# Optimization experiments

Measured on AMD Instinct MI355X. Metric: run time of the kernel, lower is better.

## Reference

```python
import jax, jax.numpy as jnp
import numpy as np

D_MODEL = 1024
N_HEADS = 16
D_HEAD = 64
D_FF = 4096
BATCH = 4
SEQ = 2048
EPS = 1e-05


def gelu_lean(x):
    cubic = x * x * x
    cdf = 0.5 * (1.0 + jnp.tanh(0.7978845608 * (x + 0.044715 * cubic)))
    return x * cdf


def layernorm(x, gamma, beta):
    mean = jnp.mean(x, axis=-1, keepdims=True)
    var = jnp.mean((x - mean) ** 2, axis=-1, keepdims=True)
    return gamma * ((x - mean) / jnp.sqrt(var + EPS)) + beta


def setup_inputs() -> dict:
    key = jax.random.key(0)
    ks = jax.random.split(key, 8)
    std = 0.02
    return {
        "x": jax.random.normal(ks[0], (BATCH, SEQ, D_MODEL), dtype=jnp.float32),
        "gamma1": jnp.ones((D_MODEL,), jnp.float32),
        "beta1": jnp.zeros((D_MODEL,), jnp.float32),
        "wq": std * jax.random.normal(ks[1], (N_HEADS, D_HEAD, D_MODEL), dtype=jnp.float32),
        "wk": std * jax.random.normal(ks[2], (N_HEADS, D_HEAD, D_MODEL), dtype=jnp.float32),
        "wv": std * jax.random.normal(ks[3], (N_HEADS, D_HEAD, D_MODEL), dtype=jnp.float32),
        "wo": std * jax.random.normal(ks[4], (D_MODEL, N_HEADS * D_HEAD), dtype=jnp.float32),
        "gamma2": jnp.ones((D_MODEL,), jnp.float32),
        "beta2": jnp.zeros((D_MODEL,), jnp.float32),
        "mlp_fc1": std * jax.random.normal(ks[5], (D_FF, D_MODEL), dtype=jnp.float32),
        "mlp_fc2": std * jax.random.normal(ks[6], (D_MODEL, D_FF), dtype=jnp.float32),
    }


def reference(x, gamma1, beta1, wq, wk, wv, wo, gamma2, beta2, mlp_fc1, mlp_fc2):
    n = layernorm(x, gamma1, beta1)  # [B,S,D]
    scale = jnp.sqrt(jnp.float32(D_HEAD))
    # per-head projections, vectorized over heads: [B,S,H,dh]
    q = jnp.einsum("bsd,hed->bshe", n, wq)
    k = jnp.einsum("bsd,hed->bshe", n, wk)
    v = jnp.einsum("bsd,hed->bshe", n, wv)
    scores = jnp.einsum("bqhe,bkhe->bhqk", q, k) / scale  # [B,H,S,S]
    seq = x.shape[1]
    mask = jnp.triu(jnp.ones((seq, seq), dtype=bool), k=1)
    scores = jnp.where(mask, jnp.float32(-1e9), scores)
    weights = jax.nn.softmax(scores, axis=-1)
    attn = jnp.einsum("bhqk,bkhe->bqhe", weights, v)  # [B,S,H,dh]
    concat = attn.reshape(x.shape[0], seq, N_HEADS * D_HEAD)  # head-order concat
    attn_out = concat @ wo.T
    x_resid = x + attn_out
    n2 = layernorm(x_resid, gamma2, beta2)
    hidden = gelu_lean(n2 @ mlp_fc1.T)
    mlp_out = hidden @ mlp_fc2.T
    return x_resid + mlp_out
```

## Files before the change

### kernel.cpp

```cpp
#include <hip/hip_runtime.h>
#include <hip/hip_bf16.h>

#define D_MODEL 1024
#define N_HEADS 16
#define D_HEAD  64
#define D_FF    4096
#define BATCH   4
#define SEQ     2048
#define ROWS    (BATCH*SEQ)
#define LN_EPS  1e-5f

typedef __bf16 bf16;
typedef __bf16 bf16x8 __attribute__((ext_vector_type(8)));
typedef float  f32x4  __attribute__((ext_vector_type(4)));

__device__ __forceinline__ void load16_lds(const bf16* g, bf16* l) {
#if defined(__has_builtin) && __has_builtin(__builtin_amdgcn_global_load_lds)
    __builtin_amdgcn_global_load_lds(
        (const __attribute__((address_space(1))) unsigned int*)g,
        (__attribute__((address_space(3))) unsigned int*)l,
        16, 0, 0);
#else
    const int lane = threadIdx.x & 63;
    ((bf16x8*)l)[lane] = *(const bf16x8*)g;
#endif
}

__global__ __launch_bounds__(256) void f2b4_kernel(const float* a, const float* b,
                                                   const float* c, const float* d,
                                                   bf16* oa, bf16* ob, bf16* oc, bf16* od,
                                                   int n) {
    const float* srcs[4] = {a, b, c, d};
    bf16* dsts[4] = {oa, ob, oc, od};
    const float* s = srcs[blockIdx.y];
    bf16* dst = dsts[blockIdx.y];
    int i = blockIdx.x * 256 + threadIdx.x;
    int stride = gridDim.x * 256;
    for (; i < n; i += stride) dst[i] = (bf16)s[i];
}
__global__ __launch_bounds__(256) void f2b2_kernel(const float* a, const float* b,
                                                   bf16* oa, bf16* ob, int n) {
    const float* s = blockIdx.y ? b : a;
    bf16* dst = blockIdx.y ? ob : oa;
    int i = blockIdx.x * 256 + threadIdx.x;
    int stride = gridDim.x * 256;
    for (; i < n; i += stride) dst[i] = (bf16)s[i];
}

__global__ __launch_bounds__(256) void ln_kernel(const float* __restrict__ x,
                                                 const float* __restrict__ gamma,
                                                 const float* __restrict__ beta,
                                                 bf16* __restrict__ out) {
    const int row = blockIdx.x;
    const int tid = threadIdx.x;
    const float* xr = x + (size_t)row * D_MODEL;

    float vals[4];
    float s = 0.f, ss = 0.f;
#pragma unroll
    for (int t = 0; t < 4; ++t) {
        float v = xr[tid + t * 256];
        vals[t] = v;
        s += v;
        ss += v * v;
    }
#pragma unroll
    for (int off = 32; off > 0; off >>= 1) {
        s  += __shfl_xor(s, off, 64);
        ss += __shfl_xor(ss, off, 64);
    }
    __shared__ float sbuf[4], ssbuf[4];
    const int wave = tid >> 6;
    if ((tid & 63) == 0) { sbuf[wave] = s; ssbuf[wave] = ss; }
    __syncthreads();
    s  = sbuf[0] + sbuf[1] + sbuf[2] + sbuf[3];
    ss = ssbuf[0] + ssbuf[1] + ssbuf[2] + ssbuf[3];

    const float mean = s * (1.f / D_MODEL);
    const float var  = ss * (1.f / D_MODEL) - mean * mean;
    const float inv  = rsqrtf(var + LN_EPS);

    bf16* orow = out + (size_t)row * D_MODEL;
#pragma unroll
    for (int t = 0; t < 4; ++t) {
        int c = tid + t * 256;
        orow[c] = (bf16)(gamma[c] * ((vals[t] - mean) * inv) + beta[c]);
    }
}

__device__ __forceinline__ float gelu_f(float x) {
    const float y = x * (0.7978845608f + 0.0356774081f * x * x);
    return x / (1.f + __expf(-2.f * y));
}

template <int EPI, int TN, int BK, typename OutT>
__global__ __launch_bounds__(256) void gemm_mt(const bf16* __restrict__ A,
                                               const bf16* __restrict__ W,
                                               OutT* C,
                                               const float* ADD,
                                               bf16* VT,
                                               int M, int N, int K, int LDK) {
    constexpr int WN = TN / 64;
    constexpr int WM = 4 / WN;
    constexpr int SM = (128 / WM) / 16;

    constexpr int AB_ELEMS = 128 * BK + TN * BK;
    constexpr int TB_ELEMS = (EPI == 4) ? 4 * 64 * 72 : 0;
    constexpr int SMEM_ELEMS = AB_ELEMS > TB_ELEMS ? AB_ELEMS : TB_ELEMS;
    __shared__ __align__(16) bf16 smem[SMEM_ELEMS];
    bf16* sA   = smem;
    bf16* sB   = smem + 128 * BK;
    bf16* tbuf = smem;

    const int wave = threadIdx.x >> 6;
    const int lane = threadIdx.x & 63;
    const int quad = lane >> 4;
    const int l16  = lane & 15;
    const int wm   = wave / WN;
    const int wn   = wave % WN;

    const int nN  = N / TN;
    const int b   = blockIdx.x;
    const int xcd = b & 7;
    const int j   = b >> 3;
    const int bx  = j % nN;
    const int band = (j / nN) * 8 + xcd;

    const int m0 = band * 128;
    const int n0 = bx * TN;

    f32x4 acc[SM][4] = {};

    if constexpr (BK == 32) {
        const int srow = lane >> 2;
        const int scol = (lane & 3) * 8;
        const bf16* gA0 = A + (size_t)(m0 + wave * 32 + srow) * LDK + scol;
        const bf16* gA1 = gA0 + (size_t)16 * LDK;
        bf16* lA0 = &sA[(wave * 32) * 32];
        bf16* lA1 = &sA[(wave * 32 + 16) * 32];
        const bf16* gB0 = W + (size_t)(n0 + wave * (TN / 4) + srow) * LDK + scol;
        const bf16* gB1 = gB0 + (size_t)16 * LDK;
        bf16* lB0 = &sB[(wave * (TN / 4)) * 32];
        bf16* lB1 = &sB[(wave * (TN / 4) + 16) * 32];

        for (int k0 = 0; k0 < K; k0 += 32) {
            load16_lds(gA0 + k0, lA0);
            load16_lds(gA1 + k0, lA1);
            load16_lds(gB0 + k0, lB0);
            if constexpr (TN == 128) load16_lds(gB1 + k0, lB1);
            __syncthreads();

            bf16x8 af[SM], bfr[4];
#pragma unroll
            for (int s = 0; s < SM; ++s)
                af[s] = *reinterpret_cast<const bf16x8*>(&sA[(wm * (128 / WM) + s * 16 + l16) * 32 + quad * 8]);
#pragma unroll
            for (int t = 0; t < 4; ++t)
                bfr[t] = *reinterpret_cast<const bf16x8*>(&sB[(wn * 64 + t * 16 + l16) * 32 + quad * 8]);
#pragma unroll
            for (int s = 0; s < SM; ++s)
#pragma unroll
                for (int t = 0; t < 4; ++t)
                    acc[s][t] = __builtin_amdgcn_mfma_f32_16x16x32_bf16(af[s], bfr[t], acc[s][t], 0, 0, 0);
            __syncthreads();
        }
    } else {
        const int lrow = lane >> 3;
        const int lch  = ((lane & 7) ^ lrow) * 8;
        const bf16* gA = A + (size_t)(m0 + wave * 32 + lrow) * LDK + lch;
        bf16* lA = &sA[(wave * 32) * 64];
        const bf16* gB = W + (size_t)(n0 + wave * (TN / 4) + lrow) * LDK + lch;
        bf16* lB = &sB[(wave * (TN / 4)) * 64];

        for (int k0 = 0; k0 < K; k0 += 64) {
#pragma unroll
            for (int i = 0; i < 4; ++i)
                load16_lds(gA + k0 + (size_t)(8 * i) * LDK, lA + 8 * i * 64);
#pragma unroll
            for (int i = 0; i < (TN / 4) / 8; ++i)
                load16_lds(gB + k0 + (size_t)(8 * i) * LDK, lB + 8 * i * 64);
            __syncthreads();

#pragma unroll
            for (int kk = 0; kk < 2; ++kk) {
                bf16x8 af[SM], bfr[4];
#pragma unroll
                for (int s = 0; s < SM; ++s) {
                    const int row = wm * (128 / WM) + s * 16 + l16;
                    const int sl  = (kk * 4 + quad) ^ (row & 7);
                    af[s] = *reinterpret_cast<const bf16x8*>(&sA[row * 64 + sl * 8]);
                }
#pragma unroll
                for (int t = 0; t < 4; ++t) {
                    const int row = wn * 64 + t * 16 + l16;
                    const int sl  = (kk * 4 + quad) ^ (row & 7);
                    bfr[t] = *reinterpret_cast<const bf16x8*>(&sB[row * 64 + sl * 8]);
                }
#pragma unroll
                for (int s = 0; s < SM; ++s)
#pragma unroll
                    for (int t = 0; t < 4; ++t)
                        acc[s][t] = __builtin_amdgcn_mfma_f32_16x16x32_bf16(af[s], bfr[t], acc[s][t], 0, 0, 0);
            }
            __syncthreads();
        }
    }

    if constexpr (EPI == 4) {
        if (n0 >= 2048) {
            bf16* tw = &tbuf[wave * 64 * 72];
#pragma unroll
            for (int s = 0; s < SM; ++s)
#pragma unroll
                for (int t = 0; t < 4; ++t)
#pragma unroll
                    for (int r = 0; r < 4; ++r)
                        tw[(t * 16 + l16) * 72 + s * 16 + quad * 4 + r] = (bf16)acc[s][t][r];
#pragma unroll
            for (int i = 0; i < 8; ++i) {
                const int flat = i * 64 + lane;
                const int nl = flat >> 3;
                const int mc = flat & 7;
                bf16x8 v = *reinterpret_cast<const bf16x8*>(&tw[nl * 72 + mc * 8]);
                const int vcol = n0 - 2048 + wn * 64 + nl;
                const int m_glob = m0 + wm * 64 + mc * 8;
                const int bb = m_glob >> 11, sp = m_glob & (SEQ - 1);
                const int hh = vcol >> 6,  dh = vcol & 63;
                const size_t tidx = (((size_t)(bb * N_HEADS + hh) * D_HEAD + dh) << 11) + sp;
                *reinterpret_cast<bf16x8*>(&VT[tidx]) = v;
            }
        } else {
            const float qscale = (n0 < 1024) ? 0.125f : 1.0f;
#pragma unroll
            for (int s = 0; s < SM; ++s) {
                const int mbase = m0 + wm * (128 / WM) + s * 16 + quad * 4;
#pragma unroll
                for (int t = 0; t < 4; ++t) {
                    const int n = n0 + wn * 64 + t * 16 + l16;
#pragma unroll
                    for (int r = 0; r < 4; ++r)
                        C[(size_t)(mbase + r) * 2048 + n] = (OutT)(acc[s][t][r] * qscale);
                }
            }
        }
    } else {
#pragma unroll
        for (int s = 0; s < SM; ++s) {
            const int mbase = m0 + wm * (128 / WM) + s * 16 + quad * 4;
#pragma unroll
            for (int t = 0; t < 4; ++t) {
                const int n = n0 + wn * 64 + t * 16 + l16;
#pragma unroll
                for (int r = 0; r < 4; ++r) {
                    float v = acc[s][t][r];
                    if (EPI == 1) v = gelu_f(v);
                    const size_t idx = (size_t)(mbase + r) * N + n;
                    if (EPI == 2) v += ADD[idx];
                    C[idx] = (OutT)v;
                }
            }
        }
    }
}

__global__ __launch_bounds__(256) void flash_attn_kernel(const bf16* __restrict__ qk,
                                                         const bf16* __restrict__ vt,
                                                         bf16* __restrict__ o) {
    const int id   = blockIdx.x;
    const int bhl  = id & 7;
    const int rest = id >> 3;
    const int pair = rest & 15;
    const int bhh  = rest >> 4;
    const int bh   = bhh * 8 + bhl;
    const int b    = bh >> 4;
    const int h    = bh & 15;
    const int wave = threadIdx.x >> 6;
    const int lane = threadIdx.x & 63;
    const int quad = lane >> 4;
    const int l16  = lane & 15;

    __shared__ __align__(16) bf16 sK[2][64 * 64];
    __shared__ __align__(16) bf16 sV[2][64 * 64];
    __shared__ bf16 pbuf[4][16][68];

    const bf16* kbase = qk + (size_t)(b * SEQ) * 2048 + 1024 + h * D_HEAD;
    const bf16* vbase = vt + ((size_t)(bh * D_HEAD) << 11);

    const int lrow   = lane >> 3;
    const int lchunk = (lane & 7) ^ lrow;
    const int xr     = l16 & 7;

    auto stage = [&](int j0, int buf) {
        const bf16* gk = kbase + (size_t)(j0 + wave * 16 + lrow) * 2048 + lchunk * 8;
        const bf16* gv = vbase + (size_t)(wave * 16 + lrow) * 2048 + j0 + lchunk * 8;
        load16_lds(gk,            &sK[buf][(wave * 16) * 64]);
        load16_lds(gk + 8 * 2048, &sK[buf][(wave * 16 + 8) * 64]);
        load16_lds(gv,            &sV[buf][(wave * 16) * 64]);
        load16_lds(gv + 8 * 2048, &sV[buf][(wave * 16 + 8) * 64]);
    };

    bf16x8 ones;
#pragma unroll
    for (int i = 0; i < 8; ++i) ones[i] = (bf16)1.0f;

    for (int half = 0; half < 2; ++half) {
        const int qtile = half ? 31 - pair : pair;
        const int q0 = qtile * 64 + wave * 16;
        const size_t qrow = (size_t)(b * SEQ + q0 + l16) * 2048 + h * D_HEAD;
        bf16x8 qf0 = *reinterpret_cast<const bf16x8*>(qk + qrow + quad * 8);
        bf16x8 qf1 = *reinterpret_cast<const bf16x8*>(qk + qrow + 32 + quad * 8);

        f32x4 o_acc[4] = {(f32x4)(0.f), (f32x4)(0.f), (f32x4)(0.f), (f32x4)(0.f)};
        float m_q = -1e30f;
        float l_r[4] = {0.f, 0.f, 0.f, 0.f};

        stage(0, 0);
        __syncthreads();

        for (int jt = 0; jt <= qtile; ++jt) {
            const int j0 = jt * 64;
            const int cur = jt & 1;
            if (jt < qtile) stage(j0 + 64, cur ^ 1);

            const bf16* sKc = sK[cur];
            const bf16* sVc = sV[cur];

            f32x4 s_acc[4] = {(f32x4)(0.f), (f32x4)(0.f), (f32x4)(0.f), (f32x4)(0.f)};
#pragma unroll
            for (int nb = 0; nb < 4; ++nb) {
                const int row = nb * 16 + l16;
                const int slot = quad ^ xr;
                bf16x8 kf0 = *reinterpret_cast<const bf16x8*>(&sKc[row * 64 + slot * 8]);
                bf16x8 kf1 = *reinterpret_cast<const bf16x8*>(&sKc[row * 64 + (slot ^ 4) * 8]);
                s_acc[nb] = __builtin_amdgcn_mfma_f32_16x16x32_bf16(qf0, kf0, s_acc[nb], 0, 0, 0);
                s_acc[nb] = __builtin_amdgcn_mfma_f32_16x16x32_bf16(qf1, kf1, s_acc[nb], 0, 0, 0);
            }
            const bool diag = (jt == qtile);
            float sv[4][4];
            float mx = -1e30f;
#pragma unroll
            for (int nb = 0; nb < 4; ++nb) {
                const int key = j0 + nb * 16 + l16;
#pragma unroll
                for (int r = 0; r < 4; ++r) {
                    float s = s_acc[nb][r];
                    if (diag && key > q0 + quad * 4 + r) s = -1e30f;
                    sv[nb][r] = s;
                    mx = fmaxf(mx, s);
                }
            }
#pragma unroll
            for (int off = 1; off < 16; off <<= 1) mx = fmaxf(mx, __shfl_xor(mx, off, 64));
            const float mn = fmaxf(m_q, mx);
            const float alpha = __expf(m_q - mn);
            m_q = mn;
#pragma unroll
            for (int nb = 0; nb < 4; ++nb)
#pragma unroll
                for (int r = 0; r < 4; ++r)
                    pbuf[wave][quad * 4 + r][nb * 16 + l16] = (bf16)__expf(sv[nb][r] - mn);
#pragma unroll
            for (int r = 0; r < 4; ++r) l_r[r] *= alpha;
#pragma unroll
            for (int nb = 0; nb < 4; ++nb) o_acc[nb] *= alpha;
            bf16x8 pf0 = *reinterpret_cast<const bf16x8*>(&pbuf[wave][l16][quad * 8]);
            bf16x8 pf1 = *reinterpret_cast<const bf16x8*>(&pbuf[wave][l16][32 + quad * 8]);
            f32x4 lt = (f32x4)(0.f);
            lt = __builtin_amdgcn_mfma_f32_16x16x32_bf16(pf0, ones, lt, 0, 0, 0);
            lt = __builtin_amdgcn_mfma_f32_16x16x32_bf16(pf1, ones, lt, 0, 0, 0);
#pragma unroll
            for (int r = 0; r < 4; ++r) l_r[r] += lt[r];
#pragma unroll
            for (int nb = 0; nb < 4; ++nb) {
                const int row = nb * 16 + l16;
                const int slot = quad ^ xr;
                bf16x8 vf0 = *reinterpret_cast<const bf16x8*>(&sVc[row * 64 + slot * 8]);
                bf16x8 vf1 = *reinterpret_cast<const bf16x8*>(&sVc[row * 64 + (slot ^ 4) * 8]);
                o_acc[nb] = __builtin_amdgcn_mfma_f32_16x16x32_bf16(pf0, vf0, o_acc[nb], 0, 0, 0);
                o_acc[nb] = __builtin_amdgcn_mfma_f32_16x16x32_bf16(pf1, vf1, o_acc[nb], 0, 0, 0);
            }
            __syncthreads();
        }
#pragma unroll
        for (int nb = 0; nb < 4; ++nb) {
#pragma unroll
            for (int r = 0; r < 4; ++r) {
                const int qrow_g = q0 + quad * 4 + r;
                o[(size_t)(b * SEQ + qrow_g) * D_MODEL + h * D_HEAD + nb * 16 + l16] =
                    (bf16)(o_acc[nb][r] / l_r[r]);
            }
        }
    }
}

extern "C" void kernel_launch(void* const* d_in, const int* in_sizes, int n_in,
                              void* d_out, int out_size, void* d_ws, size_t ws_size,
                              hipStream_t stream) {
    const float* x      = (const float*)d_in[0];
    const float* gamma1 = (const float*)d_in[1];
    const float* beta1  = (const float*)d_in[2];
    const float* wq     = (const float*)d_in[3];
    const float* wk     = (const float*)d_in[4];
    const float* wv     = (const float*)d_in[5];
    const float* wo     = (const float*)d_in[6];
    const float* gamma2 = (const float*)d_in[7];
    const float* beta2  = (const float*)d_in[8];
    const float* fc1    = (const float*)d_in[9];
    const float* fc2    = (const float*)d_in[10];
    float* out = (float*)d_out;

    const size_t WSMALL = (size_t)N_HEADS * D_HEAD * D_MODEL;
    const size_t WFF    = (size_t)D_FF * D_MODEL;
    const size_t RD     = (size_t)ROWS * D_MODEL;

    char* wsb = (char*)d_ws;
    bf16* wq_b  = (bf16*)(wsb);
    bf16* wk_b  = wq_b + WSMALL;
    bf16* wv_b  = wk_b + WSMALL;
    bf16* wo_b  = wv_b + WSMALL;
    bf16* fc1_b = wo_b + WSMALL;
    bf16* fc2_b = fc1_b + WFF;
    bf16* slotA = fc2_b + WFF;
    bf16* qkb   = slotA + RD;
    bf16* vtb   = qkb + 2 * RD;

    bf16* n1    = slotA;
    bf16* attnb = slotA;
    bf16* hid   = slotA;
    float* resid = out;

    const size_t need_single = (size_t)(24 + 64 + 16) * 1024 * 1024;
    const bool single = ws_size >= need_single;
    bf16* n2 = single ? (bf16*)(wsb + (size_t)88 * 1024 * 1024) : vtb;

    f2b4_kernel<<<dim3(64, 4), 256, 0, stream>>>(wq, wk, wv, wo, wq_b, wk_b, wv_b, wo_b, (int)WSMALL);
    f2b2_kernel<<<dim3(256, 2), 256, 0, stream>>>(fc1, fc2, fc1_b, fc2_b, (int)WFF);

    ln_kernel<<<ROWS, 256, 0, stream>>>(x, gamma1, beta1, n1);
    gemm_mt<4, 128, 64, bf16><<<(3072 / 128) * (ROWS / 128), 256, 0, stream>>>(n1, wq_b, qkb, nullptr, vtb, ROWS, 3072, D_MODEL, D_MODEL);
    flash_attn_kernel<<<1024, 256, 0, stream>>>(qkb, vtb, attnb);
    gemm_mt<2, 64, 64, float><<<(D_MODEL / 64) * (ROWS / 128), 256, 0, stream>>>(attnb, wo_b, resid, x, nullptr, ROWS, D_MODEL, D_MODEL, D_MODEL);
    ln_kernel<<<ROWS, 256, 0, stream>>>(resid, gamma2, beta2, n2);

    if (single) {
        gemm_mt<1, 128, 64, bf16><<<(D_FF / 128) * (ROWS / 128), 256, 0, stream>>>(n2, fc1_b, hid, nullptr, nullptr, ROWS, D_FF, D_MODEL, D_MODEL);
        gemm_mt<2, 64, 64, float><<<(D_MODEL / 64) * (ROWS / 128), 256, 0, stream>>>(hid, fc2_b, out, resid, nullptr, ROWS, D_MODEL, D_FF, D_FF);
    } else {
        const int CHUNK = 4096;
        for (int c = 0; c < ROWS / CHUNK; ++c) {
            const bf16*  n2c    = n2    + (size_t)c * CHUNK * D_MODEL;
            const float* residc = resid + (size_t)c * CHUNK * D_MODEL;
            float*       outc   = out   + (size_t)c * CHUNK * D_MODEL;
            gemm_mt<1, 128, 64, bf16><<<(D_FF / 128) * (CHUNK / 128), 256, 0, stream>>>(n2c, fc1_b, hid, nullptr, nullptr, CHUNK, D_FF, D_MODEL, D_MODEL);
            gemm_mt<2, 64, 64, float><<<(D_MODEL / 64) * (CHUNK / 128), 256, 0, stream>>>(hid, fc2_b, outc, residc, nullptr, CHUNK, D_MODEL, D_FF, D_FF);
        }
    }
}
```

Baseline: 546.9 us.

## Transpose attention MFMA so P stays in registers, dropping LDS round-trip

Swaps the MFMA operand order so S^T is computed, with each lane holding one query column. K rows are loaded into LDS in a permuted order so the accumulator layout matches the B-operand layout needed for the P·V MFMA. This removes the per-tile LDS write/read of P and the ones-MFMA used for row sums, which are replaced by register sums and two shuffles. Output is written as packed bf16x4 vectors. The cost is more complex index arithmetic for the causal mask and the permuted K staging.

New measurement: 527.6 us. 1.04x faster.

```diff
diff --git a/kernel.cpp b/kernel.cpp
--- a/kernel.cpp
+++ b/kernel.cpp
@@ -12,6 +12,7 @@
 
 typedef __bf16 bf16;
 typedef __bf16 bf16x8 __attribute__((ext_vector_type(8)));
+typedef __bf16 bf16x4 __attribute__((ext_vector_type(4)));
 typedef float  f32x4  __attribute__((ext_vector_type(4)));
 
 __device__ __forceinline__ void load16_lds(const bf16* g, bf16* l) {
@@ -281,7 +282,6 @@
 
     __shared__ __align__(16) bf16 sK[2][64 * 64];
     __shared__ __align__(16) bf16 sV[2][64 * 64];
-    __shared__ bf16 pbuf[4][16][68];
 
     const bf16* kbase = qk + (size_t)(b * SEQ) * 2048 + 1024 + h * D_HEAD;
     const bf16* vbase = vt + ((size_t)(bh * D_HEAD) << 11);
@@ -290,29 +290,31 @@
     const int lchunk = (lane & 7) ^ lrow;
     const int xr     = l16 & 7;
 
+    auto sig = [](int i) { return (i & 32) + (((i >> 2) & 3) << 3) + (((i >> 4) & 1) << 2) + (i & 3); };
+    const int sg0 = sig(wave * 16 + lrow);
+    const int sg1 = sig(wave * 16 + 8 + lrow);
+
     auto stage = [&](int j0, int buf) {
-        const bf16* gk = kbase + (size_t)(j0 + wave * 16 + lrow) * 2048 + lchunk * 8;
-        const bf16* gv = vbase + (size_t)(wave * 16 + lrow) * 2048 + j0 + lchunk * 8;
-        load16_lds(gk,            &sK[buf][(wave * 16) * 64]);
-        load16_lds(gk + 8 * 2048, &sK[buf][(wave * 16 + 8) * 64]);
+        const bf16* gk0 = kbase + (size_t)(j0 + sg0) * 2048 + lchunk * 8;
+        const bf16* gk1 = kbase + (size_t)(j0 + sg1) * 2048 + lchunk * 8;
+        const bf16* gv  = vbase + (size_t)(wave * 16 + lrow) * 2048 + j0 + lchunk * 8;
+        load16_lds(gk0, &sK[buf][(wave * 16) * 64]);
+        load16_lds(gk1, &sK[buf][(wave * 16 + 8) * 64]);
         load16_lds(gv,            &sV[buf][(wave * 16) * 64]);
         load16_lds(gv + 8 * 2048, &sV[buf][(wave * 16 + 8) * 64]);
     };
 
-    bf16x8 ones;
-#pragma unroll
-    for (int i = 0; i < 8; ++i) ones[i] = (bf16)1.0f;
-
     for (int half = 0; half < 2; ++half) {
         const int qtile = half ? 31 - pair : pair;
         const int q0 = qtile * 64 + wave * 16;
-        const size_t qrow = (size_t)(b * SEQ + q0 + l16) * 2048 + h * D_HEAD;
+        const int qg = q0 + l16;
+        const size_t qrow = (size_t)(b * SEQ + qg) * 2048 + h * D_HEAD;
         bf16x8 qf0 = *reinterpret_cast<const bf16x8*>(qk + qrow + quad * 8);
         bf16x8 qf1 = *reinterpret_cast<const bf16x8*>(qk + qrow + 32 + quad * 8);
 
         f32x4 o_acc[4] = {(f32x4)(0.f), (f32x4)(0.f), (f32x4)(0.f), (f32x4)(0.f)};
         float m_q = -1e30f;
-        float l_r[4] = {0.f, 0.f, 0.f, 0.f};
+        float l_r = 0.f;
 
         stage(0, 0);
         __syncthreads();
@@ -332,63 +334,77 @@
                 const int slot = quad ^ xr;
                 bf16x8 kf0 = *reinterpret_cast<const bf16x8*>(&sKc[row * 64 + slot * 8]);
                 bf16x8 kf1 = *reinterpret_cast<const bf16x8*>(&sKc[row * 64 + (slot ^ 4) * 8]);
-                s_acc[nb] = __builtin_amdgcn_mfma_f32_16x16x32_bf16(qf0, kf0, s_acc[nb], 0, 0, 0);
-                s_acc[nb] = __builtin_amdgcn_mfma_f32_16x16x32_bf16(qf1, kf1, s_acc[nb], 0, 0, 0);
-            }
+                s_acc[nb] = __builtin_amdgcn_mfma_f32_16x16x32_bf16(kf0, qf0, s_acc[nb], 0, 0, 0);
+                s_acc[nb] = __builtin_amdgcn_mfma_f32_16x16x32_bf16(kf1, qf1, s_acc[nb], 0, 0, 0);
+            }
+
             const bool diag = (jt == qtile);
-            float sv[4][4];
+            float p[4][4];
             float mx = -1e30f;
 #pragma unroll
             for (int nb = 0; nb < 4; ++nb) {
-                const int key = j0 + nb * 16 + l16;
 #pragma unroll
                 for (int r = 0; r < 4; ++r) {
                     float s = s_acc[nb][r];
-                    if (diag && key > q0 + quad * 4 + r) s = -1e30f;
-                    sv[nb][r] = s;
+                    if (diag) {
+                        const int key = j0 + ((nb & 2) << 4) + (quad << 3) + ((nb & 1) << 2) + r;
+                        if (key > qg) s = -1e30f;
+                    }
+                    p[nb][r] = s;
                     mx = fmaxf(mx, s);
                 }
             }
-#pragma unroll
-            for (int off = 1; off < 16; off <<= 1) mx = fmaxf(mx, __shfl_xor(mx, off, 64));
+            mx = fmaxf(mx, __shfl_xor(mx, 16, 64));
+            mx = fmaxf(mx, __shfl_xor(mx, 32, 64));
             const float mn = fmaxf(m_q, mx);
             const float alpha = __expf(m_q - mn);
             m_q = mn;
+
+            float ts = 0.f;
 #pragma unroll
             for (int nb = 0; nb < 4; ++nb)
 #pragma unroll
-                for (int r = 0; r < 4; ++r)
-                    pbuf[wave][quad * 4 + r][nb * 16 + l16] = (bf16)__expf(sv[nb][r] - mn);
-#pragma unroll
-            for (int r = 0; r < 4; ++r) l_r[r] *= alpha;
+                for (int r = 0; r < 4; ++r) {
+                    const float e = __expf(p[nb][r] - mn);
+                    p[nb][r] = e;
+                    ts += e;
+                }
+            ts += __shfl_xor(ts, 16, 64);
+            ts += __shfl_xor(ts, 32, 64);
+            l_r = l_r * alpha + ts;
+
+            bf16x8 pb0, pb1;
+#pragma unroll
+            for (int r = 0; r < 4; ++r) {
+                pb0[r]     = (bf16)p[0][r];
+                pb0[4 + r] = (bf16)p[1][r];
+                pb1[r]     = (bf16)p[2][r];
+                pb1[4 + r] = (bf16)p[3][r];
+            }
+
 #pragma unroll
             for (int nb = 0; nb < 4; ++nb) o_acc[nb] *= alpha;
-            bf16x8 pf0 = *reinterpret_cast<const bf16x8*>(&pbuf[wave][l16][quad * 8]);
-            bf16x8 pf1 = *reinterpret_cast<const bf16x8*>(&pbuf[wave][l16][32 + quad * 8]);
-            f32x4 lt = (f32x4)(0.f);
-            lt = __builtin_amdgcn_mfma_f32_16x16x32_bf16(pf0, ones, lt, 0, 0, 0);
-            lt = __builtin_amdgcn_mfma_f32_16x16x32_bf16(pf1, ones, lt, 0, 0, 0);
-#pragma unroll
-            for (int r = 0; r < 4; ++r) l_r[r] += lt[r];
+
 #pragma unroll
             for (int nb = 0; nb < 4; ++nb) {
                 const int row = nb * 16 + l16;
                 const int slot = quad ^ xr;
                 bf16x8 vf0 = *reinterpret_cast<const bf16x8*>(&sVc[row * 64 + slot * 8]);
                 bf16x8 vf1 = *reinterpret_cast<const bf16x8*>(&sVc[row * 64 + (slot ^ 4) * 8]);
-                o_acc[nb] = __builtin_amdgcn_mfma_f32_16x16x32_bf16(pf0, vf0, o_acc[nb], 0, 0, 0);
-                o_acc[nb] = __builtin_amdgcn_mfma_f32_16x16x32_bf16(pf1, vf1, o_acc[nb], 0, 0, 0);
+                o_acc[nb] = __builtin_amdgcn_mfma_f32_16x16x32_bf16(vf0, pb0, o_acc[nb], 0, 0, 0);
+                o_acc[nb] = __builtin_amdgcn_mfma_f32_16x16x32_bf16(vf1, pb1, o_acc[nb], 0, 0, 0);
             }
             __syncthreads();
         }
+
+        const float inv = 1.f / l_r;
 #pragma unroll
         for (int nb = 0; nb < 4; ++nb) {
-#pragma unroll
-            for (int r = 0; r < 4; ++r) {
-                const int qrow_g = q0 + quad * 4 + r;
-                o[(size_t)(b * SEQ + qrow_g) * D_MODEL + h * D_HEAD + nb * 16 + l16] =
-                    (bf16)(o_acc[nb][r] / l_r[r]);
-            }
+            bf16x4 ov;
+#pragma unroll
+            for (int r = 0; r < 4; ++r) ov[r] = (bf16)(o_acc[nb][r] * inv);
+            *reinterpret_cast<bf16x4*>(
+                &o[(size_t)(b * SEQ + qg) * D_MODEL + h * D_HEAD + nb * 16 + quad * 4]) = ov;
         }
     }
 }
```
